# Optimization experiments

Measured on AMD Instinct MI355X. Metric: run time of the kernel, lower is better.

Reference implementation:

```python
import jax, jax.numpy as jnp
import numpy as np

P, G, UV = 5, 40000, 256          # n_parts, gs_num (visible UV texels), uv_size
ZD, FD, HD = 32, 64, 32           # latent_z_dim, latent_f_dim, latent_h_dim
H1, L1 = 128, 3                   # mlp1 hidden dim, fc layers
H2, L2 = 128, 3                   # mlp2 hidden dim, fc layers
CC, LC = 64, 4                    # cnn hidden channels, cnn hidden layers


def _mlp_params(key, din, hid, nlayers, dout, nparts):
    ks = jax.random.split(key, 3)
    s = lambda f: 1.0 / np.sqrt(f)
    return dict(
        w_in=jax.random.normal(ks[0], (nparts, din, hid), jnp.float32) * s(din),
        b_in=jnp.zeros((nparts, hid), jnp.float32),
        w_hid=jax.random.normal(ks[1], (nparts, nlayers - 1, hid, hid), jnp.float32) * s(hid),
        b_hid=jnp.zeros((nparts, nlayers - 1, hid), jnp.float32),
        w_out=jax.random.normal(ks[2], (nparts, hid, dout), jnp.float32) * s(hid),
        b_out=jnp.zeros((nparts, dout), jnp.float32),
    )


def setup_inputs() -> dict:
    key = jax.random.key(0)
    ks = jax.random.split(key, 12)
    d1 = FD + ZD
    d2 = d1 + 3 + 11
    inp = {
        'latent_z': jax.random.normal(ks[2], (G, ZD), jnp.float32),
        'latent_f': jax.random.normal(ks[3], (P, FD), jnp.float32),
        'cano_xyz': jax.random.normal(ks[4], (G, 3), jnp.float32),
    }
    for k, v in _mlp_params(ks[0], d1, H1, L1, 11, P).items():
        inp['mlp1_' + k] = v
    for k, v in _mlp_params(ks[1], d2, H2, L2, HD, P).items():
        inp['mlp2_' + k] = v
    inp['conv_in_w'] = jax.random.normal(ks[5], (CC, HD, 3, 3), jnp.float32) * (1.0 / np.sqrt(HD * 9))
    inp['conv_in_b'] = jnp.zeros((CC,), jnp.float32)
    inp['conv_hid_w'] = jax.random.normal(ks[6], (LC - 1, CC, CC, 3, 3), jnp.float32) * (1.0 / np.sqrt(CC * 9))
    inp['conv_hid_b'] = jnp.zeros((LC - 1, CC), jnp.float32)
    inp['conv_out_w'] = jax.random.normal(ks[7], (3, CC, 3, 3), jnp.float32) * (1.0 / np.sqrt(CC * 9))
    inp['conv_out_b'] = jnp.zeros((3,), jnp.float32)
    inp['gs_part'] = jax.random.randint(ks[8], (G,), 0, P, jnp.int32)
    inp['uv_idx'] = jax.random.permutation(ks[9], UV * UV)[:G].astype(jnp.int32)  # unique visible texels
    return inp


def _part_mlp(x, w_in, b_in, w_hid, b_hid, w_out, b_out, part):
    # x: [G, D]; weights stacked over parts. Run every part's MLP, gather by part id.
    h = jax.nn.leaky_relu(jnp.einsum('gd,pdh->pgh', x, w_in) + b_in[:, None, :])
    for l in range(w_hid.shape[1]):
        h = jax.nn.leaky_relu(jnp.einsum('pgh,pho->pgo', h, w_hid[:, l]) + b_hid[:, l][:, None, :])
    out = jnp.einsum('pgh,pho->pgo', h, w_out) + b_out[:, None, :]  # [P, G, O]
    return out[part, jnp.arange(out.shape[1])]                       # [G, O]


def _conv(x, w, b):
    y = jax.lax.conv_general_dilated(x, w, (1, 1), 'SAME',
                                     dimension_numbers=('NCHW', 'OIHW', 'NCHW'))
    return y + b[None, :, None, None]


def _instance_norm(x, eps=1e-5):
    m = x.mean(axis=(2, 3), keepdims=True)
    v = x.var(axis=(2, 3), keepdims=True)
    return (x - m) / jnp.sqrt(v + eps)


def reference(latent_z, latent_f, cano_xyz,
              mlp1_w_in, mlp1_b_in, mlp1_w_hid, mlp1_b_hid, mlp1_w_out, mlp1_b_out,
              mlp2_w_in, mlp2_b_in, mlp2_w_hid, mlp2_b_hid, mlp2_w_out, mlp2_b_out,
              conv_in_w, conv_in_b, conv_hid_w, conv_hid_b, conv_out_w, conv_out_b,
              gs_part, uv_idx):
    feat_f = latent_f[gs_part]                                  # [G, FD] per-part feature gather
    x1 = jnp.concatenate([feat_f, latent_z], axis=-1)           # [G, FD+ZD]
    attrs = _part_mlp(x1, mlp1_w_in, mlp1_b_in, mlp1_w_hid, mlp1_b_hid,
                      mlp1_w_out, mlp1_b_out, gs_part)          # [G, 11] gaussian attrs
    x2 = jnp.concatenate([x1, cano_xyz, attrs], axis=-1)        # [G, FD+ZD+3+11]
    h = _part_mlp(x2, mlp2_w_in, mlp2_b_in, mlp2_w_hid, mlp2_b_hid,
                  mlp2_w_out, mlp2_b_out, gs_part)              # [G, HD]
    # scatter per-gaussian features back into the UV map (uvmask-indexed texels)
    uvmap = jnp.zeros((UV * UV, h.shape[-1]), h.dtype).at[uv_idx].add(h)
    x = uvmap.T.reshape(1, h.shape[-1], UV, UV)                 # [1, HD, UV, UV]
    # CNN refinement: conv -> (relu, conv, instance_norm) x (LC-1) -> conv -> sigmoid
    x = _conv(x, conv_in_w, conv_in_b)
    for l in range(conv_hid_w.shape[0]):
        x = _instance_norm(_conv(jax.nn.relu(x), conv_hid_w[l], conv_hid_b[l]))
    x = _conv(x, conv_out_w, conv_out_b)
    return jax.nn.sigmoid(x)                                    # [1, 3, UV, UV]
```

## Files before the change

### kernel.cpp

```cpp
#include <hip/hip_runtime.h>

#define G_N 40000
#define P_N 5
#define PIX 65536
#define XP 136
#define SP 32

typedef short short8 __attribute__((ext_vector_type(8)));
typedef short short4v __attribute__((ext_vector_type(4)));
typedef float f32x4 __attribute__((ext_vector_type(4)));
#define MFMA16(a, b, c) __builtin_amdgcn_mfma_f32_16x16x32_bf16(a, b, c, 0, 0, 0)

__device__ __forceinline__ short f2b(float f) {
    unsigned u = __builtin_bit_cast(unsigned, f);
    unsigned r = (u + 0x7fffu + ((u >> 16) & 1u)) >> 16;
    return (short)r;
}
__device__ __forceinline__ float b2f(short s) {
    unsigned u = ((unsigned)(unsigned short)s) << 16;
    return __builtin_bit_cast(float, u);
}


__global__ __launch_bounds__(256) void hist_k(const int* __restrict__ part,
                                              int* __restrict__ counts, int n) {
    __shared__ int s_c[P_N];
    if (threadIdx.x < P_N) s_c[threadIdx.x] = 0;
    __syncthreads();
    int g = blockIdx.x * 256 + threadIdx.x;
    if (g < n) atomicAdd(&s_c[part[g]], 1);
    __syncthreads();
    if (threadIdx.x < P_N) atomicAdd(&counts[threadIdx.x], s_c[threadIdx.x]);
}

__global__ void offs_k(const int* __restrict__ counts, int* __restrict__ offs) {
    if (threadIdx.x == 0) {
        int o = 0;
        for (int p = 0; p < P_N; ++p) {
            offs[p] = o;
            o += (counts[p] + 63) & ~63;
        }
        offs[P_N] = o;
    }
}

__global__ __launch_bounds__(256) void scatter_k(const int* __restrict__ part,
                                                 const int* __restrict__ offs,
                                                 int* __restrict__ cursors,
                                                 int* __restrict__ perm, int n) {
    const int t = threadIdx.x;
    const int g = blockIdx.x * 256 + t;
    const int p = (g < n) ? part[g] : -1;
    const int lane = t & 63;
    const int wid = t >> 6;
    __shared__ int s_wc[4][P_N];
    __shared__ int s_base[P_N];
    const unsigned long long lmask = (1ull << lane) - 1ull;
    int myrank = 0;
    for (int pp = 0; pp < P_N; ++pp) {
        unsigned long long m = __ballot(p == pp);
        if (p == pp) myrank = __popcll(m & lmask);
        if (lane == 0) s_wc[wid][pp] = __popcll(m);
    }
    __syncthreads();
    if (t < P_N) {
        int tot = s_wc[0][t] + s_wc[1][t] + s_wc[2][t] + s_wc[3][t];
        s_base[t] = atomicAdd(&cursors[t], tot);
    }
    __syncthreads();
    if (g < n) {
        int pre = 0;
        #pragma unroll
        for (int w2 = 0; w2 < 4; ++w2) if (w2 < wid) pre += s_wc[w2][p];
        perm[offs[p] + s_base[p] + pre + myrank] = g;
    }
}


__device__ __forceinline__ float mseg(int l, const float* __restrict__ src,
                                      int DIN, int DOUT, int NP, int pps) {
    const int pn = NP * 128;
    const int p = l / pn;
    const int r = l - p * pn;
    const int n = r >> 7, k = r & 127;
    return (n < DOUT && k < DIN) ? src[p * pps + k * DOUT + n] : 0.f;
}
__device__ __forceinline__ float cseg(int l, const float* __restrict__ src, int CIN) {
    const int per = 9 * 64 * CIN;
    const int ll = l / per;
    int rem = l - ll * per;
    const int tap = rem / (64 * CIN);
    rem -= tap * 64 * CIN;
    const int och = rem / CIN;
    const int ci = rem - och * CIN;
    return src[((ll * 64 + och) * CIN + ci) * 9 + tap];
}

__global__ __launch_bounds__(256) void prep_k(
        const float* __restrict__ m1wi, const float* __restrict__ m1wh,
        const float* __restrict__ m1wo, const float* __restrict__ m2wi,
        const float* __restrict__ m2wh, const float* __restrict__ m2wo,
        const float* __restrict__ cinw, const float* __restrict__ chw,
        short* __restrict__ wb) {
    const int idx = blockIdx.x * 256 + threadIdx.x;
    if (idx >= 651264) return;
    float v;
    if      (idx < 81920)  v = mseg(idx,          m1wi,         96, 128, 128, 12288);
    else if (idx < 163840) v = mseg(idx - 81920,  m1wh,        128, 128, 128, 32768);
    else if (idx < 245760) v = mseg(idx - 163840, m1wh + 16384,128, 128, 128, 32768);
    else if (idx < 256000) v = mseg(idx - 245760, m1wo,        128,  11,  16, 1408);
    else if (idx < 337920) v = mseg(idx - 256000, m2wi,        110, 128, 128, 14080);
    else if (idx < 419840) v = mseg(idx - 337920, m2wh,        128, 128, 128, 32768);
    else if (idx < 501760) v = mseg(idx - 419840, m2wh + 16384,128, 128, 128, 32768);
    else if (idx < 522240) v = mseg(idx - 501760, m2wo,        128,  32,  32, 4096);
    else if (idx < 540672) v = cseg(idx - 522240, cinw, 32);
    else                   v = cseg(idx - 540672, chw, 64);
    wb[idx] = f2b(v);
}


template<int NKC, bool ACT>
__device__ __forceinline__ void wlayer32(const short8 (&A)[2][NKC],
                                         const short* __restrict__ wt,
                                         const float* __restrict__ bias,
                                         short* dst, int ln, int lq) {
    #pragma unroll
    for (int nt = 0; nt < 8; ++nt) {
        short8 B[NKC];
        #pragma unroll
        for (int kc = 0; kc < NKC; ++kc)
            B[kc] = *(const short8*)(wt + (nt * 16 + ln) * 128 + kc * 32 + lq * 8);
        const float bs = bias[nt * 16 + ln];
        #pragma unroll
        for (int mt = 0; mt < 2; ++mt) {
            f32x4 acc = {bs, bs, bs, bs};
            #pragma unroll
            for (int kc = 0; kc < NKC; ++kc) acc = MFMA16(A[mt][kc], B[kc], acc);
            #pragma unroll
            for (int r = 0; r < 4; ++r) {
                float v = acc[r];
                if (ACT) v = fmaxf(v, 0.01f * v);
                dst[(mt * 16 + lq * 4 + r) * XP + nt * 16 + ln] = f2b(v);
            }
        }
    }
}

__device__ __forceinline__ void pre2(short8 (&A)[2][4], const short* s, int ln, int lq) {
    #pragma unroll
    for (int mt = 0; mt < 2; ++mt)
        #pragma unroll
        for (int kc = 0; kc < 4; ++kc)
            A[mt][kc] = *(const short8*)(s + (mt * 16 + ln) * XP + kc * 32 + lq * 8);
}

__global__ __launch_bounds__(128, 2) void mlp_k(
        const float* __restrict__ latent_z, const float* __restrict__ latent_f,
        const float* __restrict__ cano,
        const short* __restrict__ wt1i, const float* __restrict__ b1i,
        const short* __restrict__ wt1h0, const short* __restrict__ wt1h1,
        const float* __restrict__ b1h,
        const short* __restrict__ wt1o, const float* __restrict__ b1o,
        const short* __restrict__ wt2i, const float* __restrict__ b2i,
        const short* __restrict__ wt2h0, const short* __restrict__ wt2h1,
        const float* __restrict__ b2h,
        const short* __restrict__ wt2o, const float* __restrict__ b2o,
        const int* __restrict__ uv_idx, const int* __restrict__ perm,
        const int* __restrict__ offs, const int* __restrict__ counts,
        unsigned short* __restrict__ uvmap ) {
    __shared__ short s_h[64 * XP];
    __shared__ short s_c4[64 * SP];
    __shared__ int s_g[64];
    __shared__ int s_uv[64];

    const int t = threadIdx.x;
    const int lane = t & 63;
    const int ln = lane & 15, lq = lane >> 4;
    const int w = t >> 6;
    const int pos0 = blockIdx.x * 64;
    if (pos0 >= offs[P_N]) return;
    int p = 0;
    #pragma unroll
    for (int q = 1; q < P_N; ++q) if (pos0 >= offs[q]) p = q;
    const int vend = offs[p] + counts[p];

    if (t < 64) {
        const int pos = pos0 + t;
        const int g = (pos < vend) ? perm[pos] : -1;
        s_g[t] = g;
        s_uv[t] = (g >= 0) ? uv_idx[g] : 0;
    }
    for (int i = t; i < 64 * SP / 2; i += 128) ((int*)s_c4)[i] = 0;
    __syncthreads();

    for (int i = t; i < 64 * 16; i += 128) {
        const int g = i >> 4, k4 = (i & 15) * 4;
        const float4 v = *(const float4*)(latent_f + p * 64 + k4);
        short4v o = {f2b(v.x), f2b(v.y), f2b(v.z), f2b(v.w)};
        *(short4v*)(s_h + g * XP + k4) = o;
    }
    for (int i = t; i < 64 * 8; i += 128) {
        const int g = i >> 3, k4 = (i & 7) * 4;
        const int gg = s_g[g];
        short4v o = {0, 0, 0, 0};
        if (gg >= 0) {
            const float4 v = *(const float4*)(latent_z + gg * 32 + k4);
            o[0] = f2b(v.x); o[1] = f2b(v.y); o[2] = f2b(v.z); o[3] = f2b(v.w);
        }
        *(short4v*)(s_h + g * XP + 64 + k4) = o;
    }
    for (int i = t; i < 64 * 3; i += 128) {
        const int g = i / 3, k = i - g * 3;
        const int gg = s_g[g];
        s_c4[g * SP + k] = (gg >= 0) ? f2b(cano[gg * 3 + k]) : 0;
    }
    __syncthreads();

    short* myh = s_h + w * 32 * XP;
    short* myc = s_c4 + w * 32 * SP;
    const int gbase = w * 32;

    short8 A1[2][3];
    #pragma unroll
    for (int mt = 0; mt < 2; ++mt)
        #pragma unroll
        for (int kc = 0; kc < 3; ++kc)
            A1[mt][kc] = *(const short8*)(myh + (mt * 16 + ln) * XP + kc * 32 + lq * 8);

    wlayer32<3, true>(A1, wt1i + p * 16384, b1i + p * 128, myh, ln, lq);
    {
        short8 Ah[2][4];
        pre2(Ah, myh, ln, lq);
        wlayer32<4, true>(Ah, wt1h0 + p * 16384, b1h + (p * 2 + 0) * 128, myh, ln, lq);
        pre2(Ah, myh, ln, lq);
        wlayer32<4, true>(Ah, wt1h1 + p * 16384, b1h + (p * 2 + 1) * 128, myh, ln, lq);
        pre2(Ah, myh, ln, lq);
        short8 B[4];
        #pragma unroll
        for (int kc = 0; kc < 4; ++kc)
            B[kc] = *(const short8*)(wt1o + p * 2048 + ln * 128 + kc * 32 + lq * 8);
        const float bs = (ln < 11) ? b1o[p * 11 + ln] : 0.f;
        #pragma unroll
        for (int mt = 0; mt < 2; ++mt) {
            f32x4 acc = {bs, bs, bs, bs};
            #pragma unroll
            for (int kc = 0; kc < 4; ++kc) acc = MFMA16(Ah[mt][kc], B[kc], acc);
            if (ln < 11) {
                #pragma unroll
                for (int r = 0; r < 4; ++r)
                    myc[(mt * 16 + lq * 4 + r) * SP + 3 + ln] = f2b(acc[r]);
            }
        }
    }

    {
        short8 A2[2][4];
        #pragma unroll
        for (int mt = 0; mt < 2; ++mt) {
            A2[mt][0] = A1[mt][0]; A2[mt][1] = A1[mt][1]; A2[mt][2] = A1[mt][2];
            A2[mt][3] = *(const short8*)(myc + (mt * 16 + ln) * SP + lq * 8);
        }
        wlayer32<4, true>(A2, wt2i + p * 16384, b2i + p * 128, myh, ln, lq);
    }
    {
        short8 Ah[2][4];
        pre2(Ah, myh, ln, lq);
        wlayer32<4, true>(Ah, wt2h0 + p * 16384, b2h + (p * 2 + 0) * 128, myh, ln, lq);
        pre2(Ah, myh, ln, lq);
        wlayer32<4, true>(Ah, wt2h1 + p * 16384, b2h + (p * 2 + 1) * 128, myh, ln, lq);
        pre2(Ah, myh, ln, lq);
        #pragma unroll
        for (int nt = 0; nt < 2; ++nt) {
            short8 B[4];
            #pragma unroll
            for (int kc = 0; kc < 4; ++kc)
                B[kc] = *(const short8*)(wt2o + p * 4096 + (nt * 16 + ln) * 128 + kc * 32 + lq * 8);
            const float bs = b2o[p * 32 + nt * 16 + ln];
            #pragma unroll
            for (int mt = 0; mt < 2; ++mt) {
                f32x4 acc = {bs, bs, bs, bs};
                #pragma unroll
                for (int kc = 0; kc < 4; ++kc) acc = MFMA16(Ah[mt][kc], B[kc], acc);
                #pragma unroll
                for (int r = 0; r < 4; ++r) {
                    const int m = gbase + mt * 16 + lq * 4 + r;
                    if (s_g[m] >= 0)
                        uvmap[s_uv[m] * 32 + nt * 16 + ln] = (unsigned short)f2b(acc[r]);
                }
            }
        }
    }
}


template<int CIN, int TRANS, bool STATS>
__global__ __launch_bounds__(256, 2) void conv_k(
        const unsigned short* __restrict__ in,
        const short* __restrict__ wt,
        const float* __restrict__ bias,
        const float* __restrict__ psum, const float* __restrict__ psq,
        unsigned short* __restrict__ out,
        float* __restrict__ ssum, float* __restrict__ ssq) {
    constexpr int CS = CIN + 8;
    constexpr int NKC = CIN / 32;
    constexpr int RUNS = CIN / 8;
    __shared__ short s_in[10 * 18 * CS];
    __shared__ float s_mr[2][64];
    __shared__ float s_red[4][2][64];

    const int t = threadIdx.x;
    const int lane = t & 63;
    const int ln = lane & 15, lq = lane >> 4;
    const int w4 = t >> 6;
    const int tx0 = blockIdx.x * 16, ty0 = blockIdx.y * 8;

    if (TRANS == 2 && t < 64) {
        const float m = psum[t] * (1.f / PIX);
        const float vv = psq[t] * (1.f / PIX) - m * m;
        s_mr[0][t] = m;
        s_mr[1][t] = rsqrtf(vv + 1e-5f);
    }
    if (TRANS == 2) __syncthreads();

    for (int i = t; i < 180 * RUNS; i += 256) {
        const int sp = i / RUNS, run = i - sp * RUNS;
        const int r = sp / 18, c = sp - r * 18;
        const int gy = ty0 + r - 1, gx = tx0 + c - 1;
        short* dst = &s_in[(r * 18 + c) * CS + run * 8];
        if (gy >= 0 && gy < 256 && gx >= 0 && gx < 256) {
            short8 v = *(const short8*)(in + ((gy * 256 + gx) * CIN + run * 8));
            if (TRANS == 0) {
                *(short8*)dst = v;
            } else {
                short8 o;
                #pragma unroll
                for (int j = 0; j < 8; ++j) {
                    float f = b2f(v[j]);
                    if (TRANS == 2) f = (f - s_mr[0][run * 8 + j]) * s_mr[1][run * 8 + j];
                    o[j] = f2b(fmaxf(f, 0.f));
                }
                *(short8*)dst = o;
            }
        } else {
            short8 z = {0, 0, 0, 0, 0, 0, 0, 0};
            *(short8*)dst = z;
        }
    }
    __syncthreads();

    f32x4 acc[2][4];
    {
        float bs[4];
        #pragma unroll
        for (int nt = 0; nt < 4; ++nt) bs[nt] = bias[nt * 16 + ln];
        #pragma unroll
        for (int mt = 0; mt < 2; ++mt)
            #pragma unroll
            for (int nt = 0; nt < 4; ++nt) {
                f32x4 a = {bs[nt], bs[nt], bs[nt], bs[nt]};
                acc[mt][nt] = a;
            }
    }

    const int r0 = w4 * 2;
    #pragma unroll
    for (int tap = 0; tap < 9; ++tap) {
        const int dy = tap / 3, dx = tap - dy * 3;
        const short* wtap = wt + tap * 64 * CIN;
        short8 Bc[NKC][4];
        #pragma unroll
        for (int kc = 0; kc < NKC; ++kc)
            #pragma unroll
            for (int nt = 0; nt < 4; ++nt)
                Bc[kc][nt] = *(const short8*)(wtap + (nt * 16 + ln) * CIN + kc * 32 + lq * 8);
        #pragma unroll
        for (int kc = 0; kc < NKC; ++kc) {
            short8 A[2];
            #pragma unroll
            for (int mt = 0; mt < 2; ++mt)
                A[mt] = *(const short8*)&s_in[((r0 + mt + dy) * 18 + ln + dx) * CS + kc * 32 + lq * 8];
            #pragma unroll
            for (int mt = 0; mt < 2; ++mt)
                #pragma unroll
                for (int nt = 0; nt < 4; ++nt)
                    acc[mt][nt] = MFMA16(A[mt], Bc[kc][nt], acc[mt][nt]);
        }
    }

    #pragma unroll
    for (int nt = 0; nt < 4; ++nt) {
        float ls = 0.f, lsq = 0.f;
        #pragma unroll
        for (int mt = 0; mt < 2; ++mt) {
            const int gy = ty0 + r0 + mt;
            #pragma unroll
            for (int r = 0; r < 4; ++r) {
                const float v = acc[mt][nt][r];
                const int gx = tx0 + lq * 4 + r;
                out[(gy * 256 + gx) * 64 + nt * 16 + ln] = (unsigned short)f2b(v);
                if (STATS) { ls += v; lsq = fmaf(v, v, lsq); }
            }
        }
        if (STATS) {
            ls  += __shfl_xor(ls, 16, 64);
            ls  += __shfl_xor(ls, 32, 64);
            lsq += __shfl_xor(lsq, 16, 64);
            lsq += __shfl_xor(lsq, 32, 64);
            if (lane < 16) {
                s_red[w4][0][nt * 16 + ln] = ls;
                s_red[w4][1][nt * 16 + ln] = lsq;
            }
        }
    }
    if (STATS) {
        __syncthreads();
        if (t < 64) {
            atomicAdd(&ssum[t], s_red[0][0][t] + s_red[1][0][t] + s_red[2][0][t] + s_red[3][0][t]);
            atomicAdd(&ssq[t],  s_red[0][1][t] + s_red[1][1][t] + s_red[2][1][t] + s_red[3][1][t]);
        }
    }
}

__global__ __launch_bounds__(128) void convout_k(
        const unsigned short* __restrict__ in,
        const float* __restrict__ w,
        const float* __restrict__ bias,
        const float* __restrict__ psum, const float* __restrict__ psq,
        float* __restrict__ out) {
    constexpr int CS = 72;
    __shared__ short s_in[10 * 18 * CS];
    __shared__ float s_w[3][9][64];
    __shared__ float s_mr[2][64];

    const int t = threadIdx.x;
    const int tx0 = blockIdx.x * 16, ty0 = blockIdx.y * 8;
    if (t < 64) {
        const float m = psum[t] * (1.f / PIX);
        const float vv = psq[t] * (1.f / PIX) - m * m;
        s_mr[0][t] = m;
        s_mr[1][t] = rsqrtf(vv + 1e-5f);
    }
    __syncthreads();

    for (int i = t; i < 180 * 8; i += 128) {
        const int sp = i >> 3, run = i & 7;
        const int r = sp / 18, c = sp - r * 18;
        const int gy = ty0 + r - 1, gx = tx0 + c - 1;
        short* dst = &s_in[(r * 18 + c) * CS + run * 8];
        if (gy >= 0 && gy < 256 && gx >= 0 && gx < 256) {
            short8 v = *(const short8*)(in + ((gy * 256 + gx) * 64 + run * 8));
            short8 o;
            #pragma unroll
            for (int j = 0; j < 8; ++j) {
                const float f = (b2f(v[j]) - s_mr[0][run * 8 + j]) * s_mr[1][run * 8 + j];
                o[j] = f2b(f);
            }
            *(short8*)dst = o;
        } else {
            short8 z = {0, 0, 0, 0, 0, 0, 0, 0};
            *(short8*)dst = z;
        }
    }
    for (int i = t; i < 1728; i += 128) {
        const int o = i / 576;
        const int rem = i - o * 576;
        const int tap = rem >> 6;
        const int ci = rem & 63;
        s_w[o][tap][ci] = w[o * 576 + ci * 9 + tap];
    }
    __syncthreads();

    const int py = t >> 4, px = t & 15;
    float a0 = bias[0], a1 = bias[1], a2 = bias[2];
    for (int tap = 0; tap < 9; ++tap) {
        const int dy = tap / 3, dx = tap % 3;
        const short* rp = &s_in[((py + dy) * 18 + (px + dx)) * CS];
        #pragma unroll
        for (int c8 = 0; c8 < 8; ++c8) {
            short8 v = *(const short8*)(rp + c8 * 8);
            #pragma unroll
            for (int j = 0; j < 8; ++j) {
                const float f = b2f(v[j]);
                const int ci = c8 * 8 + j;
                a0 = fmaf(f, s_w[0][tap][ci], a0);
                a1 = fmaf(f, s_w[1][tap][ci], a1);
                a2 = fmaf(f, s_w[2][tap][ci], a2);
            }
        }
    }
    const int pix = (ty0 + py) * 256 + tx0 + px;
    out[pix]           = 1.f / (1.f + expf(-a0));
    out[PIX + pix]     = 1.f / (1.f + expf(-a1));
    out[2 * PIX + pix] = 1.f / (1.f + expf(-a2));
}


extern "C" void kernel_launch(void* const* d_in, const int* in_sizes, int n_in,
                              void* d_out, int out_size, void* d_ws, size_t ws_size,
                              hipStream_t stream) {
    (void)in_sizes; (void)n_in; (void)out_size; (void)ws_size;
    const float* latent_z = (const float*)d_in[0];
    const float* latent_f = (const float*)d_in[1];
    const float* cano     = (const float*)d_in[2];
    const float* m1wi = (const float*)d_in[3];
    const float* m1bi = (const float*)d_in[4];
    const float* m1wh = (const float*)d_in[5];
    const float* m1bh = (const float*)d_in[6];
    const float* m1wo = (const float*)d_in[7];
    const float* m1bo = (const float*)d_in[8];
    const float* m2wi = (const float*)d_in[9];
    const float* m2bi = (const float*)d_in[10];
    const float* m2wh = (const float*)d_in[11];
    const float* m2bh = (const float*)d_in[12];
    const float* m2wo = (const float*)d_in[13];
    const float* m2bo = (const float*)d_in[14];
    const float* cinw = (const float*)d_in[15];
    const float* cinb = (const float*)d_in[16];
    const float* chw  = (const float*)d_in[17];
    const float* chb  = (const float*)d_in[18];
    const float* cow  = (const float*)d_in[19];
    const float* cob  = (const float*)d_in[20];
    const int* gs_part = (const int*)d_in[21];
    const int* uv_idx  = (const int*)d_in[22];

    float* ws = (float*)d_ws;
    unsigned short* actA = (unsigned short*)ws;
    unsigned short* actB = (unsigned short*)(ws + 2097152);
    unsigned short* uvmap = actB;

    short* wb = (short*)(ws + 4194304);
    short* wt1i  = wb;
    short* wt1h0 = wb + 81920;
    short* wt1h1 = wb + 163840;
    short* wt1o  = wb + 245760;
    short* wt2i  = wb + 256000;
    short* wt2h0 = wb + 337920;
    short* wt2h1 = wb + 419840;
    short* wt2o  = wb + 501760;
    short* cwt_in  = wb + 522240;
    short* cwt_hid = wb + 540672;

    float* small = ws + 4194304 + 330000;
    int* counts  = (int*)small;
    int* cursors = counts + 8;
    int* offs    = cursors + 8;
    float* ssum  = small + 32;
    float* ssq   = ssum + 192;
    int* perm    = (int*)(ssq + 192);

    hipMemsetAsync(uvmap, 0, (size_t)PIX * 32 * sizeof(unsigned short), stream);
    hipMemsetAsync(small, 0, 1024 * sizeof(float), stream);

    hist_k<<<157, 256, 0, stream>>>(gs_part, counts, G_N);
    offs_k<<<1, 64, 0, stream>>>(counts, offs);
    scatter_k<<<157, 256, 0, stream>>>(gs_part, offs, cursors, perm, G_N);

    prep_k<<<2544, 256, 0, stream>>>(m1wi, m1wh, m1wo, m2wi, m2wh, m2wo, cinw, chw, wb);

    mlp_k<<<630, 128, 0, stream>>>(latent_z, latent_f, cano,
        wt1i, m1bi, wt1h0, wt1h1, m1bh, wt1o, m1bo,
        wt2i, m2bi, wt2h0, wt2h1, m2bh, wt2o, m2bo,
        uv_idx, perm, offs, counts, uvmap);

    dim3 cgrid(16, 32);
    conv_k<32, 0, false><<<cgrid, 256, 0, stream>>>(uvmap, cwt_in, cinb,
        nullptr, nullptr, actA, nullptr, nullptr);
    conv_k<64, 1, true><<<cgrid, 256, 0, stream>>>(actA, cwt_hid, chb,
        nullptr, nullptr, actB, ssum, ssq);
    conv_k<64, 2, true><<<cgrid, 256, 0, stream>>>(actB, cwt_hid + 36864, chb + 64,
        ssum, ssq, actA, ssum + 64, ssq + 64);
    conv_k<64, 2, true><<<cgrid, 256, 0, stream>>>(actA, cwt_hid + 73728, chb + 128,
        ssum + 64, ssq + 64, actB, ssum + 128, ssq + 128);
    convout_k<<<cgrid, 128, 0, stream>>>(actB, cow, cob,
        ssum + 128, ssq + 128, (float*)d_out);
}
```

Measured before the change: 283.5 us.

## Stage MLP weights in LDS, swap MFMA operands, split conv output channels

The MLP kernel now copies each layer's weights and biases into shared memory before use, with barriers between layers. It swaps the MFMA operand order so each lane writes four contiguous outputs as a vector store. The conv kernels move to 128-thread blocks with a z-dimension that splits the 64 output channels into two halves, and each wave covers four rows instead of two. This doubles the block count and cuts per-thread registers, but every block now reloads the input halo tile, and the MLP kernel adds 32KB of LDS plus extra barriers.

Result: slower. 303.5 us (+7.1%).

```diff
diff --git a/kernel.cpp b/kernel.cpp
--- a/kernel.cpp
+++ b/kernel.cpp
@@ -119,39 +119,50 @@
 }
 
 
-template<int NKC, bool ACT>
-__device__ __forceinline__ void wlayer32(const short8 (&A)[2][NKC],
-                                         const short* __restrict__ wt,
-                                         const float* __restrict__ bias,
-                                         short* dst, int ln, int lq) {
+__device__ __forceinline__ void stageW(const short* __restrict__ wt,
+                                       short* s_w, int nchunks, int t) {
+    for (int idx = t; idx < nchunks; idx += 128) {
+        const int lane = idx & 63;
+        const int ln = lane & 15, lq = lane >> 4;
+        const int ntkc = idx >> 6;
+        const int nt = ntkc >> 2, kc = ntkc & 3;
+        *(short8*)(s_w + idx * 8) =
+            *(const short8*)(wt + (nt * 16 + ln) * 128 + kc * 32 + lq * 8);
+    }
+}
+
+__device__ __forceinline__ void pre2(short8 (&X)[2][4], const short* s, int ln, int lq) {
+    #pragma unroll
+    for (int mt = 0; mt < 2; ++mt)
+        #pragma unroll
+        for (int kc = 0; kc < 4; ++kc)
+            X[mt][kc] = *(const short8*)(s + (mt * 16 + ln) * XP + kc * 32 + lq * 8);
+}
+
+template<bool ACT>
+__device__ __forceinline__ void wlayerS(const short8 (&X)[2][4],
+                                        const short* s_w, const float* s_bias,
+                                        short* myh, int ln, int lq) {
     #pragma unroll
     for (int nt = 0; nt < 8; ++nt) {
-        short8 B[NKC];
-        #pragma unroll
-        for (int kc = 0; kc < NKC; ++kc)
-            B[kc] = *(const short8*)(wt + (nt * 16 + ln) * 128 + kc * 32 + lq * 8);
-        const float bs = bias[nt * 16 + ln];
+        short8 W[4];
+        #pragma unroll
+        for (int kc = 0; kc < 4; ++kc)
+            W[kc] = *(const short8*)(s_w + ((nt * 4 + kc) * 64 + lq * 16 + ln) * 8);
+        const f32x4 b4 = *(const f32x4*)(s_bias + nt * 16 + lq * 4);
         #pragma unroll
         for (int mt = 0; mt < 2; ++mt) {
-            f32x4 acc = {bs, bs, bs, bs};
-            #pragma unroll
-            for (int kc = 0; kc < NKC; ++kc) acc = MFMA16(A[mt][kc], B[kc], acc);
-            #pragma unroll
-            for (int r = 0; r < 4; ++r) {
-                float v = acc[r];
-                if (ACT) v = fmaxf(v, 0.01f * v);
-                dst[(mt * 16 + lq * 4 + r) * XP + nt * 16 + ln] = f2b(v);
-            }
-        }
-    }
-}
-
-__device__ __forceinline__ void pre2(short8 (&A)[2][4], const short* s, int ln, int lq) {
-    #pragma unroll
-    for (int mt = 0; mt < 2; ++mt)
-        #pragma unroll
-        for (int kc = 0; kc < 4; ++kc)
-            A[mt][kc] = *(const short8*)(s + (mt * 16 + ln) * XP + kc * 32 + lq * 8);
+            f32x4 acc = b4;
+            #pragma unroll
+            for (int kc = 0; kc < 4; ++kc) acc = MFMA16(W[kc], X[mt][kc], acc);
+            if (ACT) {
+                #pragma unroll
+                for (int r = 0; r < 4; ++r) acc[r] = fmaxf(acc[r], 0.01f * acc[r]);
+            }
+            short4v o = {f2b(acc[0]), f2b(acc[1]), f2b(acc[2]), f2b(acc[3])};
+            *(short4v*)(myh + (mt * 16 + ln) * XP + nt * 16 + lq * 4) = o;
+        }
+    }
 }
 
 __global__ __launch_bounds__(128, 2) void mlp_k(
@@ -169,6 +180,8 @@
         const int* __restrict__ offs, const int* __restrict__ counts,
         unsigned short* __restrict__ uvmap ) {
     __shared__ short s_h[64 * XP];
+    __shared__ short s_w[16384];
+    __shared__ float s_bias[128];
     __shared__ short s_c4[64 * SP];
     __shared__ int s_g[64];
     __shared__ int s_uv[64];
@@ -209,83 +222,124 @@
         }
         *(short4v*)(s_h + g * XP + 64 + k4) = o;
     }
+    for (int i = t; i < 64 * 8; i += 128) {
+        const int g = i >> 3, k4 = 96 + (i & 7) * 4;
+        short4v z = {0, 0, 0, 0};
+        *(short4v*)(s_h + g * XP + k4) = z;
+    }
     for (int i = t; i < 64 * 3; i += 128) {
         const int g = i / 3, k = i - g * 3;
         const int gg = s_g[g];
         s_c4[g * SP + k] = (gg >= 0) ? f2b(cano[gg * 3 + k]) : 0;
     }
+    stageW(wt1i + p * 16384, s_w, 2048, t);
+    s_bias[t] = b1i[p * 128 + t];
     __syncthreads();
 
     short* myh = s_h + w * 32 * XP;
     short* myc = s_c4 + w * 32 * SP;
     const int gbase = w * 32;
 
-    short8 A1[2][3];
-    #pragma unroll
-    for (int mt = 0; mt < 2; ++mt)
-        #pragma unroll
-        for (int kc = 0; kc < 3; ++kc)
-            A1[mt][kc] = *(const short8*)(myh + (mt * 16 + ln) * XP + kc * 32 + lq * 8);
-
-    wlayer32<3, true>(A1, wt1i + p * 16384, b1i + p * 128, myh, ln, lq);
-    {
-        short8 Ah[2][4];
-        pre2(Ah, myh, ln, lq);
-        wlayer32<4, true>(Ah, wt1h0 + p * 16384, b1h + (p * 2 + 0) * 128, myh, ln, lq);
-        pre2(Ah, myh, ln, lq);
-        wlayer32<4, true>(Ah, wt1h1 + p * 16384, b1h + (p * 2 + 1) * 128, myh, ln, lq);
-        pre2(Ah, myh, ln, lq);
-        short8 B[4];
+    short8 X1[2][4];
+    pre2(X1, myh, ln, lq);
+
+    wlayerS<true>(X1, s_w, s_bias, myh, ln, lq);
+    __syncthreads();
+    stageW(wt1h0 + p * 16384, s_w, 2048, t);
+    s_bias[t] = b1h[(p * 2 + 0) * 128 + t];
+    __syncthreads();
+    {
+        short8 X[2][4];
+        pre2(X, myh, ln, lq);
+        wlayerS<true>(X, s_w, s_bias, myh, ln, lq);
+    }
+    __syncthreads();
+    stageW(wt1h1 + p * 16384, s_w, 2048, t);
+    s_bias[t] = b1h[(p * 2 + 1) * 128 + t];
+    __syncthreads();
+    {
+        short8 X[2][4];
+        pre2(X, myh, ln, lq);
+        wlayerS<true>(X, s_w, s_bias, myh, ln, lq);
+    }
+    __syncthreads();
+    stageW(wt1o + p * 2048, s_w, 256, t);
+    if (t < 16) s_bias[t] = (t < 11) ? b1o[p * 11 + t] : 0.f;
+    __syncthreads();
+    {
+        short8 X[2][4];
+        pre2(X, myh, ln, lq);
+        short8 W[4];
         #pragma unroll
         for (int kc = 0; kc < 4; ++kc)
-            B[kc] = *(const short8*)(wt1o + p * 2048 + ln * 128 + kc * 32 + lq * 8);
-        const float bs = (ln < 11) ? b1o[p * 11 + ln] : 0.f;
+            W[kc] = *(const short8*)(s_w + (kc * 64 + lq * 16 + ln) * 8);
+        const f32x4 b4 = *(const f32x4*)(s_bias + lq * 4);
         #pragma unroll
         for (int mt = 0; mt < 2; ++mt) {
-            f32x4 acc = {bs, bs, bs, bs};
-            #pragma unroll
-            for (int kc = 0; kc < 4; ++kc) acc = MFMA16(Ah[mt][kc], B[kc], acc);
-            if (ln < 11) {
+            f32x4 acc = b4;
+            #pragma unroll
+            for (int kc = 0; kc < 4; ++kc) acc = MFMA16(W[kc], X[mt][kc], acc);
+            #pragma unroll
+            for (int r = 0; r < 4; ++r) {
+                const int n = lq * 4 + r;
+                if (n < 11) myc[(mt * 16 + ln) * SP + 3 + n] = f2b(acc[r]);
+            }
+        }
+    }
+    __syncthreads();
+    stageW(wt2i + p * 16384, s_w, 2048, t);
+    s_bias[t] = b2i[p * 128 + t];
+    __syncthreads();
+    {
+        short8 X[2][4];
+        #pragma unroll
+        for (int mt = 0; mt < 2; ++mt) {
+            X[mt][0] = X1[mt][0]; X[mt][1] = X1[mt][1]; X[mt][2] = X1[mt][2];
+            X[mt][3] = *(const short8*)(myc + (mt * 16 + ln) * SP + lq * 8);
+        }
+        wlayerS<true>(X, s_w, s_bias, myh, ln, lq);
+    }
+    __syncthreads();
+    stageW(wt2h0 + p * 16384, s_w, 2048, t);
+    s_bias[t] = b2h[(p * 2 + 0) * 128 + t];
+    __syncthreads();
+    {
+        short8 X[2][4];
+        pre2(X, myh, ln, lq);
+        wlayerS<true>(X, s_w, s_bias, myh, ln, lq);
+    }
+    __syncthreads();
+    stageW(wt2h1 + p * 16384, s_w, 2048, t);
+    s_bias[t] = b2h[(p * 2 + 1) * 128 + t];
+    __syncthreads();
+    {
+        short8 X[2][4];
+        pre2(X, myh, ln, lq);
+        wlayerS<true>(X, s_w, s_bias, myh, ln, lq);
+    }
+    __syncthreads();
+    stageW(wt2o + p * 4096, s_w, 512, t);
+    if (t < 32) s_bias[t] = b2o[p * 32 + t];
+    __syncthreads();
+    {
+        short8 X[2][4];
+        pre2(X, myh, ln, lq);
+        #pragma unroll
+        for (int nt = 0; nt < 2; ++nt) {
+            short8 W[4];
+            #pragma unroll
+            for (int kc = 0; kc < 4; ++kc)
+                W[kc] = *(const short8*)(s_w + ((nt * 4 + kc) * 64 + lq * 16 + ln) * 8);
+            const f32x4 b4 = *(const f32x4*)(s_bias + nt * 16 + lq * 4);
+            #pragma unroll
+            for (int mt = 0; mt < 2; ++mt) {
+                f32x4 acc = b4;
                 #pragma unroll
-                for (int r = 0; r < 4; ++r)
-                    myc[(mt * 16 + lq * 4 + r) * SP + 3 + ln] = f2b(acc[r]);
-            }
-        }
-    }
-
-    {
-        short8 A2[2][4];
-        #pragma unroll
-        for (int mt = 0; mt < 2; ++mt) {
-            A2[mt][0] = A1[mt][0]; A2[mt][1] = A1[mt][1]; A2[mt][2] = A1[mt][2];
-            A2[mt][3] = *(const short8*)(myc + (mt * 16 + ln) * SP + lq * 8);
-        }
-        wlayer32<4, true>(A2, wt2i + p * 16384, b2i + p * 128, myh, ln, lq);
-    }
-    {
-        short8 Ah[2][4];
-        pre2(Ah, myh, ln, lq);
-        wlayer32<4, true>(Ah, wt2h0 + p * 16384, b2h + (p * 2 + 0) * 128, myh, ln, lq);
-        pre2(Ah, myh, ln, lq);
-        wlayer32<4, true>(Ah, wt2h1 + p * 16384, b2h + (p * 2 + 1) * 128, myh, ln, lq);
-        pre2(Ah, myh, ln, lq);
-        #pragma unroll
-        for (int nt = 0; nt < 2; ++nt) {
-            short8 B[4];
-            #pragma unroll
-            for (int kc = 0; kc < 4; ++kc)
-                B[kc] = *(const short8*)(wt2o + p * 4096 + (nt * 16 + ln) * 128 + kc * 32 + lq * 8);
-            const float bs = b2o[p * 32 + nt * 16 + ln];
-            #pragma unroll
-            for (int mt = 0; mt < 2; ++mt) {
-                f32x4 acc = {bs, bs, bs, bs};
-                #pragma unroll
-                for (int kc = 0; kc < 4; ++kc) acc = MFMA16(Ah[mt][kc], B[kc], acc);
-                #pragma unroll
-                for (int r = 0; r < 4; ++r) {
-                    const int m = gbase + mt * 16 + lq * 4 + r;
-                    if (s_g[m] >= 0)
-                        uvmap[s_uv[m] * 32 + nt * 16 + ln] = (unsigned short)f2b(acc[r]);
+                for (int kc = 0; kc < 4; ++kc) acc = MFMA16(W[kc], X[mt][kc], acc);
+                const int g = gbase + mt * 16 + ln;
+                if (s_g[g] >= 0) {
+                    short4v o = {f2b(acc[0]), f2b(acc[1]), f2b(acc[2]), f2b(acc[3])};
+                    *(short4v*)((short*)uvmap + s_uv[g] * 32 + nt * 16 + lq * 4) = o;
                 }
             }
         }
@@ -294,7 +348,7 @@
 
 
 template<int CIN, int TRANS, bool STATS>
-__global__ __launch_bounds__(256, 2) void conv_k(
+__global__ __launch_bounds__(128, 2) void conv_k(
         const unsigned short* __restrict__ in,
         const short* __restrict__ wt,
         const float* __restrict__ bias,
@@ -306,13 +360,14 @@
     constexpr int RUNS = CIN / 8;
     __shared__ short s_in[10 * 18 * CS];
     __shared__ float s_mr[2][64];
-    __shared__ float s_red[4][2][64];
+    __shared__ float s_red[2][2][32];
 
     const int t = threadIdx.x;
     const int lane = t & 63;
     const int ln = lane & 15, lq = lane >> 4;
-    const int w4 = t >> 6;
+    const int w2 = t >> 6;
     const int tx0 = blockIdx.x * 16, ty0 = blockIdx.y * 8;
+    const int och0 = blockIdx.z * 32;
 
     if (TRANS == 2 && t < 64) {
         const float m = psum[t] * (1.f / PIX);
@@ -322,7 +377,7 @@
     }
     if (TRANS == 2) __syncthreads();
 
-    for (int i = t; i < 180 * RUNS; i += 256) {
+    for (int i = t; i < 180 * RUNS; i += 128) {
         const int sp = i / RUNS, run = i - sp * RUNS;
         const int r = sp / 18, c = sp - r * 18;
         const int gy = ty0 + r - 1, gx = tx0 + c - 1;
@@ -348,56 +403,56 @@
     }
     __syncthreads();
 
-    f32x4 acc[2][4];
-    {
-        float bs[4];
-        #pragma unroll
-        for (int nt = 0; nt < 4; ++nt) bs[nt] = bias[nt * 16 + ln];
-        #pragma unroll
-        for (int mt = 0; mt < 2; ++mt)
-            #pragma unroll
-            for (int nt = 0; nt < 4; ++nt) {
+    f32x4 acc[4][2];
+    {
+        float bs[2];
+        #pragma unroll
+        for (int nt = 0; nt < 2; ++nt) bs[nt] = bias[och0 + nt * 16 + ln];
+        #pragma unroll
+        for (int mt = 0; mt < 4; ++mt)
+            #pragma unroll
+            for (int nt = 0; nt < 2; ++nt) {
                 f32x4 a = {bs[nt], bs[nt], bs[nt], bs[nt]};
                 acc[mt][nt] = a;
             }
     }
 
-    const int r0 = w4 * 2;
+    const int r0 = w2 * 4;
     #pragma unroll
     for (int tap = 0; tap < 9; ++tap) {
         const int dy = tap / 3, dx = tap - dy * 3;
         const short* wtap = wt + tap * 64 * CIN;
-        short8 Bc[NKC][4];
+        short8 Bc[NKC][2];
         #pragma unroll
         for (int kc = 0; kc < NKC; ++kc)
             #pragma unroll
-            for (int nt = 0; nt < 4; ++nt)
-                Bc[kc][nt] = *(const short8*)(wtap + (nt * 16 + ln) * CIN + kc * 32 + lq * 8);
+            for (int nt = 0; nt < 2; ++nt)
+                Bc[kc][nt] = *(const short8*)(wtap + (och0 + nt * 16 + ln) * CIN + kc * 32 + lq * 8);
         #pragma unroll
         for (int kc = 0; kc < NKC; ++kc) {
-            short8 A[2];
-            #pragma unroll
-            for (int mt = 0; mt < 2; ++mt)
+            short8 A[4];
+            #pragma unroll
+            for (int mt = 0; mt < 4; ++mt)
                 A[mt] = *(const short8*)&s_in[((r0 + mt + dy) * 18 + ln + dx) * CS + kc * 32 + lq * 8];
             #pragma unroll
-            for (int mt = 0; mt < 2; ++mt)
+            for (int mt = 0; mt < 4; ++mt)
                 #pragma unroll
-                for (int nt = 0; nt < 4; ++nt)
+                for (int nt = 0; nt < 2; ++nt)
                     acc[mt][nt] = MFMA16(A[mt], Bc[kc][nt], acc[mt][nt]);
         }
     }
 
     #pragma unroll
-    for (int nt = 0; nt < 4; ++nt) {
+    for (int nt = 0; nt < 2; ++nt) {
         float ls = 0.f, lsq = 0.f;
         #pragma unroll
-        for (int mt = 0; mt < 2; ++mt) {
+        for (int mt = 0; mt < 4; ++mt) {
             const int gy = ty0 + r0 + mt;
             #pragma unroll
             for (int r = 0; r < 4; ++r) {
                 const float v = acc[mt][nt][r];
                 const int gx = tx0 + lq * 4 + r;
-                out[(gy * 256 + gx) * 64 + nt * 16 + ln] = (unsigned short)f2b(v);
+                out[(gy * 256 + gx) * 64 + och0 + nt * 16 + ln] = (unsigned short)f2b(v);
                 if (STATS) { ls += v; lsq = fmaf(v, v, lsq); }
             }
         }
@@ -407,16 +462,16 @@
             lsq += __shfl_xor(lsq, 16, 64);
             lsq += __shfl_xor(lsq, 32, 64);
             if (lane < 16) {
-                s_red[w4][0][nt * 16 + ln] = ls;
-                s_red[w4][1][nt * 16 + ln] = lsq;
+                s_red[w2][0][nt * 16 + ln] = ls;
+                s_red[w2][1][nt * 16 + ln] = lsq;
             }
         }
     }
     if (STATS) {
         __syncthreads();
-        if (t < 64) {
-            atomicAdd(&ssum[t], s_red[0][0][t] + s_red[1][0][t] + s_red[2][0][t] + s_red[3][0][t]);
-            atomicAdd(&ssq[t],  s_red[0][1][t] + s_red[1][1][t] + s_red[2][1][t] + s_red[3][1][t]);
+        if (t < 32) {
+            atomicAdd(&ssum[och0 + t], s_red[0][0][t] + s_red[1][0][t]);
+            atomicAdd(&ssq[och0 + t],  s_red[0][1][t] + s_red[1][1][t]);
         }
     }
 }
@@ -562,15 +617,15 @@
         wt2i, m2bi, wt2h0, wt2h1, m2bh, wt2o, m2bo,
         uv_idx, perm, offs, counts, uvmap);
 
-    dim3 cgrid(16, 32);
-    conv_k<32, 0, false><<<cgrid, 256, 0, stream>>>(uvmap, cwt_in, cinb,
+    dim3 cgrid(16, 32, 2);
+    conv_k<32, 0, false><<<cgrid, 128, 0, stream>>>(uvmap, cwt_in, cinb,
         nullptr, nullptr, actA, nullptr, nullptr);
-    conv_k<64, 1, true><<<cgrid, 256, 0, stream>>>(actA, cwt_hid, chb,
+    conv_k<64, 1, true><<<cgrid, 128, 0, stream>>>(actA, cwt_hid, chb,
         nullptr, nullptr, actB, ssum, ssq);
-    conv_k<64, 2, true><<<cgrid, 256, 0, stream>>>(actB, cwt_hid + 36864, chb + 64,
+    conv_k<64, 2, true><<<cgrid, 128, 0, stream>>>(actB, cwt_hid + 36864, chb + 64,
         ssum, ssq, actA, ssum + 64, ssq + 64);
-    conv_k<64, 2, true><<<cgrid, 256, 0, stream>>>(actA, cwt_hid + 73728, chb + 128,
+    conv_k<64, 2, true><<<cgrid, 128, 0, stream>>>(actA, cwt_hid + 73728, chb + 128,
         ssum + 64, ssq + 64, actB, ssum + 128, ssq + 128);
-    convout_k<<<cgrid, 128, 0, stream>>>(actB, cow, cob,
+    convout_k<<<dim3(16, 32), 128, 0, stream>>>(actB, cow, cob,
         ssum + 128, ssq + 128, (float*)d_out);
 }
```
